# Kernel tuning notes

Measured on AMD Instinct MI355X. Metric: run time of the kernel, lower is better.

Reference implementation:

```python
import jax, jax.numpy as jnp
import numpy as np

DIM = 640
HEADS = 10
HEAD_DIM = DIM // HEADS
SCALE = DIM ** (-0.5)  # note: module scales by full dim**-0.5, not head_dim


def setup_inputs() -> dict:
    key = jax.random.key(0)
    ks = jax.random.split(key, 5)
    B, N = 16, 1024
    x = jax.random.normal(ks[0], (B, N, DIM), dtype=jnp.float32)
    w_qkv = jax.random.normal(ks[1], (DIM, 3 * DIM), dtype=jnp.float32) * (DIM ** -0.5)
    b_qkv = jnp.zeros((3 * DIM,), dtype=jnp.float32)
    w_out = jax.random.normal(ks[2], (DIM, DIM), dtype=jnp.float32) * (DIM ** -0.5)
    b_out = jnp.zeros((DIM,), dtype=jnp.float32)
    return {"x": x, "w_qkv": w_qkv, "b_qkv": b_qkv, "w_out": w_out, "b_out": b_out}


def reference(x, w_qkv, b_qkv, w_out, b_out):
    B, N, _ = x.shape
    qkv = x @ w_qkv + b_qkv                     # [B, N, 3*DIM]
    qkv = qkv.reshape(B, N, 3, HEADS, HEAD_DIM)
    q, k, v = qkv[:, :, 0], qkv[:, :, 1], qkv[:, :, 2]   # [B, N, H, Dh]
    # scores: QK^T scaled by dim**-0.5 (module's normfactor)
    scores = jnp.einsum('bihd,bjhd->bhij', q, k) * SCALE  # [B, H, N, N]
    attn = jax.nn.softmax(scores, axis=-1)
    out = jnp.einsum('bhij,bjhd->bihd', attn, v)          # [B, N, H, Dh]
    out = out.reshape(B, N, DIM)
    return out @ w_out + b_out
```

## Files before the change

kernel.cpp:

```cpp
#include <hip/hip_runtime.h>

#define DIM 640
#define NHEADS 10
#define HDIM 64
#define SEQ 1024
#define BATCH 16
#define MROWS (BATCH * SEQ)
#define QKVN (3 * DIM)
#define NBH (BATCH * NHEADS)

typedef float f32x4 __attribute__((ext_vector_type(4)));
typedef __bf16 bf16x8 __attribute__((ext_vector_type(8)));
typedef short s16x4 __attribute__((ext_vector_type(4)));

#define SM_C 0.057027536f

__device__ __forceinline__ unsigned short f2b(float f) {
  union { __bf16 h; unsigned short u; } v;
  v.h = (__bf16)f;
  return v.u;
}

__device__ __forceinline__ f32x4 mfma16(bf16x8 a, bf16x8 b, f32x4 c) {
  return __builtin_amdgcn_mfma_f32_16x16x32_bf16(a, b, c, 0, 0, 0);
}
__device__ __forceinline__ f32x4 mfma1k(s16x4 a, s16x4 b, f32x4 c) {
  return __builtin_amdgcn_mfma_f32_16x16x16bf16_1k(a, b, c, 0, 0, 0);
}

typedef __attribute__((address_space(3))) unsigned int as3_u32;
typedef const __attribute__((address_space(1))) unsigned int as1_u32;
__device__ __forceinline__ void glds16(const unsigned short* g, unsigned short* l) {
  __builtin_amdgcn_global_load_lds((as1_u32*)g, (as3_u32*)l, 16, 0, 0);
}

__global__ __launch_bounds__(256) void convert_x(
    const float* __restrict__ X, unsigned short* __restrict__ xb) {
  int i = (blockIdx.x * 256 + threadIdx.x) * 4;
  float4 v = *(const float4*)(X + i);
  ushort4 s;
  s.x = f2b(v.x); s.y = f2b(v.y); s.z = f2b(v.z); s.w = f2b(v.w);
  *(ushort4*)(xb + i) = s;
}

__global__ __launch_bounds__(256) void transpose_w(
    const float* __restrict__ W, unsigned short* __restrict__ Wt, int R, int C) {
  __shared__ int tile[32][33];
  const int tx = threadIdx.x & 31, ty = threadIdx.x >> 5;
  const int c0 = blockIdx.x * 32, r0 = blockIdx.y * 32;
#pragma unroll
  for (int i = 0; i < 4; ++i)
    tile[ty + 8 * i][tx] = f2b(W[(r0 + ty + 8 * i) * C + c0 + tx]);
  __syncthreads();
#pragma unroll
  for (int i = 0; i < 4; ++i)
    Wt[(c0 + ty + 8 * i) * R + r0 + tx] = (unsigned short)tile[tx][ty + 8 * i];
}

__global__ __launch_bounds__(256) void qkv_gemm(
    const unsigned short* __restrict__ A, const unsigned short* __restrict__ Bt,
    const float* __restrict__ bias,
    unsigned short* __restrict__ qw, unsigned short* __restrict__ kw,
    unsigned short* __restrict__ vtw) {
  __shared__ __attribute__((aligned(16))) unsigned short As[128 * 64];
  __shared__ __attribute__((aligned(16))) unsigned short Bs[128 * 64];
  const int t = threadIdx.x;
  const int lane = t & 63, w = t >> 6;
  const int quad = lane >> 4, cl = lane & 15;
  const int m0 = blockIdx.y * 128, n0 = blockIdx.x * 128;
  const int wr = (w >> 1) * 64, wc = (w & 1) * 64;

  const int r8 = lane >> 3;
  const int sw = ((lane & 7) ^ r8) * 8;
  const unsigned short* asrc = A + (size_t)(m0 + w * 32 + r8) * DIM + sw;
  const unsigned short* bsrc = Bt + (size_t)(n0 + w * 32 + r8) * DIM + sw;

  const int x = cl & 7;
  const int aoff0 = (wr + cl) * 64 + (quad ^ x) * 8;
  const int aoff1 = (wr + cl) * 64 + ((4 + quad) ^ x) * 8;
  const int boff0 = (wc + cl) * 64 + (quad ^ x) * 8;
  const int boff1 = (wc + cl) * 64 + ((4 + quad) ^ x) * 8;

  f32x4 acc[4][4];
#pragma unroll
  for (int i = 0; i < 4; ++i)
#pragma unroll
    for (int j = 0; j < 4; ++j) acc[i][j] = (f32x4){0.f, 0.f, 0.f, 0.f};

  for (int kt = 0; kt < DIM / 64; ++kt) {
    __syncthreads();
#pragma unroll
    for (int i = 0; i < 4; ++i) {
      glds16(asrc + (size_t)i * 8 * DIM, &As[(w * 32 + i * 8) * 64]);
      glds16(bsrc + (size_t)i * 8 * DIM, &Bs[(w * 32 + i * 8) * 64]);
    }
    asrc += 64; bsrc += 64;
    __syncthreads();
#pragma unroll
    for (int ks = 0; ks < 2; ++ks) {
      const int ao = ks ? aoff1 : aoff0, bo = ks ? boff1 : boff0;
      bf16x8 af[4], bfr[4];
#pragma unroll
      for (int i = 0; i < 4; ++i) af[i] = *(const bf16x8*)&As[ao + i * 1024];
#pragma unroll
      for (int j = 0; j < 4; ++j) bfr[j] = *(const bf16x8*)&Bs[bo + j * 1024];
#pragma unroll
      for (int i = 0; i < 4; ++i)
#pragma unroll
        for (int j = 0; j < 4; ++j) acc[i][j] = mfma16(af[i], bfr[j], acc[i][j]);
    }
  }

  const int sec = n0 / DIM;
  unsigned short* qk = (sec == 0) ? qw : kw;
  const float sc = (sec == 0) ? SM_C : 1.0f;
#pragma unroll
  for (int j = 0; j < 4; ++j) {
    int cc = n0 + wc + j * 16 + cl;
    int cr = cc - sec * DIM;
    int h = cr >> 6, d = cr & 63;
    float bv = bias[cc];
#pragma unroll
    for (int i = 0; i < 4; ++i) {
      int rbase = m0 + wr + i * 16 + quad * 4;
      int b = rbase >> 10, n = rbase & 1023;
      int bh = b * NHEADS + h;
      if (sec < 2) {
        size_t base = ((size_t)bh * SEQ + n) * HDIM + d;
#pragma unroll
        for (int r = 0; r < 4; ++r)
          qk[base + (size_t)r * HDIM] = f2b((acc[i][j][r] + bv) * sc);
      } else {
        ushort4 s;
        s.x = f2b(acc[i][j][0] + bv);
        s.y = f2b(acc[i][j][1] + bv);
        s.z = f2b(acc[i][j][2] + bv);
        s.w = f2b(acc[i][j][3] + bv);
        *(ushort4*)(vtw + ((size_t)bh * HDIM + d) * SEQ + n) = s;
      }
    }
  }
}

__global__ __launch_bounds__(256) void attn_kernel(
    const unsigned short* __restrict__ qw, const unsigned short* __restrict__ kw,
    const unsigned short* __restrict__ vtw, unsigned short* __restrict__ out) {
  __shared__ __attribute__((aligned(16))) unsigned short Ks[2][64 * 64];
  __shared__ __attribute__((aligned(16))) unsigned short Vs[2][64 * 64];
  const int t = threadIdx.x;
  const int lane = t & 63, w = t >> 6;
  const int quad = lane >> 4, cl = lane & 15;
  const int flat = blockIdx.x;
  const int bh = flat % NBH;
  const int qb = flat / NBH;
  const size_t qkbase = (size_t)bh * SEQ * HDIM;
  const size_t vbase  = (size_t)bh * HDIM * SEQ;

  const int r8 = lane >> 3;
  const int sw = ((lane & 7) ^ r8) * 8;
  const unsigned short* ksrc = kw + qkbase + (size_t)(w * 16 + r8) * HDIM + sw;
  const unsigned short* vsrc = vtw + vbase + (size_t)(w * 16 + r8) * SEQ + sw;

  const int x = cl & 7;
  const int koff0 = cl * 64 + (quad ^ x) * 8;
  const int koff1 = cl * 64 + ((4 + quad) ^ x) * 8;

  bf16x8 aq[2][2];
#pragma unroll
  for (int i = 0; i < 2; ++i) {
    const unsigned short* qp =
        qw + qkbase + (size_t)(qb * 128 + w * 32 + i * 16 + cl) * HDIM;
    aq[i][0] = *(const bf16x8*)(qp + quad * 8);
    aq[i][1] = *(const bf16x8*)(qp + 32 + quad * 8);
  }

  const s16x4 ones4 = {0x3F80, 0x3F80, 0x3F80, 0x3F80};

  f32x4 o_acc[2][4];
#pragma unroll
  for (int i = 0; i < 2; ++i)
#pragma unroll
    for (int dt = 0; dt < 4; ++dt) o_acc[i][dt] = (f32x4){0.f, 0.f, 0.f, 0.f};
  f32x4 o1[2];
  o1[0] = (f32x4){0.f, 0.f, 0.f, 0.f};
  o1[1] = (f32x4){0.f, 0.f, 0.f, 0.f};

  glds16(ksrc,            &Ks[0][(w * 16) * 64]);
  glds16(ksrc + 8 * HDIM, &Ks[0][(w * 16 + 8) * 64]);
  glds16(vsrc,            &Vs[0][(w * 16) * 64]);
  glds16(vsrc + 8 * SEQ,  &Vs[0][(w * 16 + 8) * 64]);

  for (int kt = 0; kt < 16; ++kt) {
    const int cur = kt & 1, nxt = cur ^ 1;
    __syncthreads();

    if (kt < 15) {
      const unsigned short* kp = ksrc + (size_t)(kt + 1) * 64 * HDIM;
      const unsigned short* vp = vsrc + (kt + 1) * 64;
      glds16(kp,            &Ks[nxt][(w * 16) * 64]);
      glds16(kp + 8 * HDIM, &Ks[nxt][(w * 16 + 8) * 64]);
      glds16(vp,            &Vs[nxt][(w * 16) * 64]);
      glds16(vp + 8 * SEQ,  &Vs[nxt][(w * 16 + 8) * 64]);
    }

    const unsigned short* Kc = &Ks[cur][0];
    const unsigned short* Vc = &Vs[cur][0];

    s16x4 pf[2][4];
#pragma unroll
    for (int jj = 0; jj < 4; ++jj) {
      bf16x8 bk0 = *(const bf16x8*)&Kc[koff0 + jj * 1024];
      bf16x8 bk1 = *(const bf16x8*)&Kc[koff1 + jj * 1024];
#pragma unroll
      for (int i = 0; i < 2; ++i) {
        f32x4 z = (f32x4){0.f, 0.f, 0.f, 0.f};
        z = mfma16(bk0, aq[i][0], z);
        z = mfma16(bk1, aq[i][1], z);
        s16x4 p;
#pragma unroll
        for (int r = 0; r < 4; ++r)
          p[r] = (short)f2b(__builtin_amdgcn_exp2f(z[r]));
        pf[i][jj] = p;
        o1[i] = mfma1k(p, ones4, o1[i]);
      }
    }

#pragma unroll
    for (int dt = 0; dt < 4; ++dt) {
      const int vrow = dt * 16 + cl;
      const int vbase_off = vrow * 64 + (quad & 1) * 4;
      const int vxor = vrow & 7;
#pragma unroll
      for (int jj = 0; jj < 4; ++jj) {
        s16x4 bv = *(const s16x4*)
            &Vc[vbase_off + ((2 * jj + (quad >> 1)) ^ vxor) * 8];
#pragma unroll
        for (int i = 0; i < 2; ++i)
          o_acc[i][dt] = mfma1k(pf[i][jj], bv, o_acc[i][dt]);
      }
    }
  }

  const int b = bh / NHEADS, h = bh % NHEADS;
#pragma unroll
  for (int i = 0; i < 2; ++i)
#pragma unroll
    for (int r = 0; r < 4; ++r) {
      float inv = 1.f / o1[i][r];
      int row = b * SEQ + qb * 128 + w * 32 + i * 16 + quad * 4 + r;
#pragma unroll
      for (int dt = 0; dt < 4; ++dt)
        out[(size_t)row * DIM + h * HDIM + dt * 16 + cl] =
            f2b(o_acc[i][dt][r] * inv);
    }
}

__global__ __launch_bounds__(256) void out_gemm(
    const unsigned short* __restrict__ A, const unsigned short* __restrict__ Bt,
    const float* __restrict__ bias, float* __restrict__ C) {
  __shared__ __attribute__((aligned(16))) unsigned short As[128 * 64];
  __shared__ __attribute__((aligned(16))) unsigned short Bs[128 * 64];
  const int t = threadIdx.x;
  const int lane = t & 63, w = t >> 6;
  const int quad = lane >> 4, cl = lane & 15;
  const int m0 = blockIdx.y * 128, n0 = blockIdx.x * 128;
  const int wr = (w >> 1) * 64, wc = (w & 1) * 64;

  const int r8 = lane >> 3;
  const int sw = ((lane & 7) ^ r8) * 8;
  const unsigned short* asrc = A + (size_t)(m0 + w * 32 + r8) * DIM + sw;
  const unsigned short* bsrc = Bt + (size_t)(n0 + w * 32 + r8) * DIM + sw;

  const int x = cl & 7;
  const int aoff0 = (wr + cl) * 64 + (quad ^ x) * 8;
  const int aoff1 = (wr + cl) * 64 + ((4 + quad) ^ x) * 8;
  const int boff0 = (wc + cl) * 64 + (quad ^ x) * 8;
  const int boff1 = (wc + cl) * 64 + ((4 + quad) ^ x) * 8;

  f32x4 acc[4][4];
#pragma unroll
  for (int i = 0; i < 4; ++i)
#pragma unroll
    for (int j = 0; j < 4; ++j) acc[i][j] = (f32x4){0.f, 0.f, 0.f, 0.f};

  for (int kt = 0; kt < DIM / 64; ++kt) {
    __syncthreads();
#pragma unroll
    for (int i = 0; i < 4; ++i) {
      glds16(asrc + (size_t)i * 8 * DIM, &As[(w * 32 + i * 8) * 64]);
      glds16(bsrc + (size_t)i * 8 * DIM, &Bs[(w * 32 + i * 8) * 64]);
    }
    asrc += 64; bsrc += 64;
    __syncthreads();
#pragma unroll
    for (int ks = 0; ks < 2; ++ks) {
      const int ao = ks ? aoff1 : aoff0, bo = ks ? boff1 : boff0;
      bf16x8 af[4], bfr[4];
#pragma unroll
      for (int i = 0; i < 4; ++i) af[i] = *(const bf16x8*)&As[ao + i * 1024];
#pragma unroll
      for (int j = 0; j < 4; ++j) bfr[j] = *(const bf16x8*)&Bs[bo + j * 1024];
#pragma unroll
      for (int i = 0; i < 4; ++i)
#pragma unroll
        for (int j = 0; j < 4; ++j) acc[i][j] = mfma16(af[i], bfr[j], acc[i][j]);
    }
  }
#pragma unroll
  for (int j = 0; j < 4; ++j) {
    int cc = n0 + wc + j * 16 + cl;
    float bv = bias[cc];
#pragma unroll
    for (int i = 0; i < 4; ++i) {
#pragma unroll
      for (int r = 0; r < 4; ++r) {
        int rr = m0 + wr + i * 16 + quad * 4 + r;
        C[(size_t)rr * DIM + cc] = acc[i][j][r] + bv;
      }
    }
  }
}

extern "C" void kernel_launch(void* const* d_in, const int* in_sizes, int n_in,
                              void* d_out, int out_size, void* d_ws, size_t ws_size,
                              hipStream_t stream) {
  const float* x     = (const float*)d_in[0];
  const float* w_qkv = (const float*)d_in[1];
  const float* b_qkv = (const float*)d_in[2];
  const float* w_out = (const float*)d_in[3];
  const float* b_out = (const float*)d_in[4];
  float* out = (float*)d_out;

  unsigned short* ws = (unsigned short*)d_ws;
  unsigned short* xb      = ws;
  unsigned short* wt_qkv  = ws + 10485760;
  unsigned short* wt_out  = wt_qkv + 1228800;
  unsigned short* qw      = wt_out + 409600;
  unsigned short* kw      = qw + 10485760;
  unsigned short* vtw     = kw + 10485760;
  unsigned short* attn_ws = xb;

  convert_x<<<MROWS * DIM / 1024, 256, 0, stream>>>(x, xb);
  transpose_w<<<dim3(QKVN / 32, DIM / 32), 256, 0, stream>>>(w_qkv, wt_qkv, DIM, QKVN);
  transpose_w<<<dim3(DIM / 32, DIM / 32), 256, 0, stream>>>(w_out, wt_out, DIM, DIM);
  qkv_gemm<<<dim3(QKVN / 128, MROWS / 128), 256, 0, stream>>>(xb, wt_qkv, b_qkv, qw, kw, vtw);
  attn_kernel<<<dim3(NBH * (SEQ / 128)), 256, 0, stream>>>(qw, kw, vtw, attn_ws);
  out_gemm<<<dim3(DIM / 128, MROWS / 128), 256, 0, stream>>>(attn_ws, wt_out, b_out, out);
}
```

Measured before the change: 258.0 us.

## Use 16x16x32 bf16 MFMA for PV by remapping K row order

Permutes the order in which K rows are loaded into shared memory so that two score tiles' exponentials pack into one bf16x8 operand matching the K=32 layout. The PV product and the row-sum then use the wider 16x16x32 MFMA instead of the 16x16x16 variant, halving instruction count for those steps and using 16-byte V reads. The risk is correctness of the remap and extra register pressure from holding two score tiles at once.

Result: faster. 244.3 us (-5.3%).

```diff
diff --git a/kernel.cpp b/kernel.cpp
--- a/kernel.cpp
+++ b/kernel.cpp
@@ -11,7 +11,6 @@
 
 typedef float f32x4 __attribute__((ext_vector_type(4)));
 typedef __bf16 bf16x8 __attribute__((ext_vector_type(8)));
-typedef short s16x4 __attribute__((ext_vector_type(4)));
 
 #define SM_C 0.057027536f
 
@@ -24,14 +23,15 @@
 __device__ __forceinline__ f32x4 mfma16(bf16x8 a, bf16x8 b, f32x4 c) {
   return __builtin_amdgcn_mfma_f32_16x16x32_bf16(a, b, c, 0, 0, 0);
 }
-__device__ __forceinline__ f32x4 mfma1k(s16x4 a, s16x4 b, f32x4 c) {
-  return __builtin_amdgcn_mfma_f32_16x16x16bf16_1k(a, b, c, 0, 0, 0);
-}
 
 typedef __attribute__((address_space(3))) unsigned int as3_u32;
 typedef const __attribute__((address_space(1))) unsigned int as1_u32;
 __device__ __forceinline__ void glds16(const unsigned short* g, unsigned short* l) {
   __builtin_amdgcn_global_load_lds((as1_u32*)g, (as3_u32*)l, 16, 0, 0);
+}
+
+__device__ __forceinline__ int kv_remap(int y) {
+  return 32 * (y >> 5) + 8 * ((y & 15) >> 2) + (y & 3) + 4 * ((y >> 4) & 1);
 }
 
 __global__ __launch_bounds__(256) void convert_x(
@@ -158,8 +158,11 @@
 
   const int r8 = lane >> 3;
   const int sw = ((lane & 7) ^ r8) * 8;
-  const unsigned short* ksrc = kw + qkbase + (size_t)(w * 16 + r8) * HDIM + sw;
-  const unsigned short* vsrc = vtw + vbase + (size_t)(w * 16 + r8) * SEQ + sw;
+  const int y0 = w * 16 + r8;
+  const int y1 = w * 16 + 8 + r8;
+  const unsigned short* ksrc0 = kw + qkbase + (size_t)kv_remap(y0) * HDIM + sw;
+  const unsigned short* ksrc1 = kw + qkbase + (size_t)kv_remap(y1) * HDIM + sw;
+  const unsigned short* vsrc  = vtw + vbase + (size_t)(w * 16 + r8) * SEQ + sw;
 
   const int x = cl & 7;
   const int koff0 = cl * 64 + (quad ^ x) * 8;
@@ -174,7 +177,10 @@
     aq[i][1] = *(const bf16x8*)(qp + 32 + quad * 8);
   }
 
-  const s16x4 ones4 = {0x3F80, 0x3F80, 0x3F80, 0x3F80};
+  union { unsigned short u[8]; bf16x8 v; } ow;
+#pragma unroll
+  for (int j = 0; j < 8; ++j) ow.u[j] = 0x3F80;
+  const bf16x8 ones8 = ow.v;
 
   f32x4 o_acc[2][4];
 #pragma unroll
@@ -185,58 +191,64 @@
   o1[0] = (f32x4){0.f, 0.f, 0.f, 0.f};
   o1[1] = (f32x4){0.f, 0.f, 0.f, 0.f};
 
-  glds16(ksrc,            &Ks[0][(w * 16) * 64]);
-  glds16(ksrc + 8 * HDIM, &Ks[0][(w * 16 + 8) * 64]);
-  glds16(vsrc,            &Vs[0][(w * 16) * 64]);
-  glds16(vsrc + 8 * SEQ,  &Vs[0][(w * 16 + 8) * 64]);
+  glds16(ksrc0, &Ks[0][(w * 16) * 64]);
+  glds16(ksrc1, &Ks[0][(w * 16 + 8) * 64]);
+  glds16(vsrc,           &Vs[0][(w * 16) * 64]);
+  glds16(vsrc + 8 * SEQ, &Vs[0][(w * 16 + 8) * 64]);
 
   for (int kt = 0; kt < 16; ++kt) {
     const int cur = kt & 1, nxt = cur ^ 1;
     __syncthreads();
 
     if (kt < 15) {
-      const unsigned short* kp = ksrc + (size_t)(kt + 1) * 64 * HDIM;
-      const unsigned short* vp = vsrc + (kt + 1) * 64;
-      glds16(kp,            &Ks[nxt][(w * 16) * 64]);
-      glds16(kp + 8 * HDIM, &Ks[nxt][(w * 16 + 8) * 64]);
-      glds16(vp,            &Vs[nxt][(w * 16) * 64]);
-      glds16(vp + 8 * SEQ,  &Vs[nxt][(w * 16 + 8) * 64]);
+      const unsigned short* kp0 = ksrc0 + (size_t)(kt + 1) * 64 * HDIM;
+      const unsigned short* kp1 = ksrc1 + (size_t)(kt + 1) * 64 * HDIM;
+      const unsigned short* vp  = vsrc + (kt + 1) * 64;
+      glds16(kp0, &Ks[nxt][(w * 16) * 64]);
+      glds16(kp1, &Ks[nxt][(w * 16 + 8) * 64]);
+      glds16(vp,           &Vs[nxt][(w * 16) * 64]);
+      glds16(vp + 8 * SEQ, &Vs[nxt][(w * 16 + 8) * 64]);
     }
 
     const unsigned short* Kc = &Ks[cur][0];
     const unsigned short* Vc = &Vs[cur][0];
 
-    s16x4 pf[2][4];
-#pragma unroll
-    for (int jj = 0; jj < 4; ++jj) {
-      bf16x8 bk0 = *(const bf16x8*)&Kc[koff0 + jj * 1024];
-      bf16x8 bk1 = *(const bf16x8*)&Kc[koff1 + jj * 1024];
+    bf16x8 pfr[2][2];
+#pragma unroll
+    for (int c = 0; c < 2; ++c) {
+      bf16x8 ka0 = *(const bf16x8*)&Kc[koff0 + c * 2048];
+      bf16x8 ka1 = *(const bf16x8*)&Kc[koff1 + c * 2048];
+      bf16x8 kb0 = *(const bf16x8*)&Kc[koff0 + c * 2048 + 1024];
+      bf16x8 kb1 = *(const bf16x8*)&Kc[koff1 + c * 2048 + 1024];
 #pragma unroll
       for (int i = 0; i < 2; ++i) {
-        f32x4 z = (f32x4){0.f, 0.f, 0.f, 0.f};
-        z = mfma16(bk0, aq[i][0], z);
-        z = mfma16(bk1, aq[i][1], z);
-        s16x4 p;
-#pragma unroll
-        for (int r = 0; r < 4; ++r)
-          p[r] = (short)f2b(__builtin_amdgcn_exp2f(z[r]));
-        pf[i][jj] = p;
-        o1[i] = mfma1k(p, ones4, o1[i]);
+        f32x4 zA = (f32x4){0.f, 0.f, 0.f, 0.f};
+        zA = mfma16(ka0, aq[i][0], zA);
+        zA = mfma16(ka1, aq[i][1], zA);
+        f32x4 zB = (f32x4){0.f, 0.f, 0.f, 0.f};
+        zB = mfma16(kb0, aq[i][0], zB);
+        zB = mfma16(kb1, aq[i][1], zB);
+        union { unsigned short u[8]; bf16x8 v; } pk;
+#pragma unroll
+        for (int r = 0; r < 4; ++r) {
+          pk.u[r]     = f2b(__builtin_amdgcn_exp2f(zA[r]));
+          pk.u[4 + r] = f2b(__builtin_amdgcn_exp2f(zB[r]));
+        }
+        pfr[i][c] = pk.v;
+        o1[i] = mfma16(pfr[i][c], ones8, o1[i]);
       }
     }
 
 #pragma unroll
     for (int dt = 0; dt < 4; ++dt) {
       const int vrow = dt * 16 + cl;
-      const int vbase_off = vrow * 64 + (quad & 1) * 4;
-      const int vxor = vrow & 7;
-#pragma unroll
-      for (int jj = 0; jj < 4; ++jj) {
-        s16x4 bv = *(const s16x4*)
-            &Vc[vbase_off + ((2 * jj + (quad >> 1)) ^ vxor) * 8];
+      const int vx = vrow & 7;
+#pragma unroll
+      for (int c = 0; c < 2; ++c) {
+        bf16x8 bv = *(const bf16x8*)&Vc[vrow * 64 + ((4 * c + quad) ^ vx) * 8];
 #pragma unroll
         for (int i = 0; i < 2; ++i)
-          o_acc[i][dt] = mfma1k(pf[i][jj], bv, o_acc[i][dt]);
+          o_acc[i][dt] = mfma16(pfr[i][c], bv, o_acc[i][dt]);
       }
     }
   }
```
